# Kernel tuning notes

Measured on AMD Instinct MI355X. Metric: run time of the kernel, lower is better.

Reference implementation:

```python
import jax, jax.numpy as jnp
import numpy as np

N, E, D, A, G, S, NG = 100000, 1600000, 64, 64, 64, 4, 16


def setup_inputs() -> dict:
    key = jax.random.key(0)
    ks = jax.random.split(key, 16)
    x = jax.random.normal(ks[0], (N, D), dtype=jnp.float32)
    x_global = jax.random.normal(ks[1], (NG, G), dtype=jnp.float32)
    edge_attr = jax.random.normal(ks[2], (E, 2), dtype=jnp.float32)
    edge_index = jax.random.randint(ks[3], (2, E), 0, N, dtype=jnp.int32)
    batch_ind = jnp.sort(jax.random.randint(ks[4], (N,), 0, NG, dtype=jnp.int32))
    s = lambda fan: 1.0 / np.sqrt(fan)
    Wm = jax.random.normal(ks[5], (S, D, A), dtype=jnp.float32) * s(D)
    bm = jnp.zeros((S, A), dtype=jnp.float32)
    Wa = jax.random.normal(ks[6], (S, D + G + A, D), dtype=jnp.float32) * s(D + G + A)
    ba = jnp.zeros((S, D), dtype=jnp.float32)
    Wgate = jax.random.normal(ks[7], (S, D, 1), dtype=jnp.float32) * s(D)
    bgate = jnp.zeros((S, 1), dtype=jnp.float32)
    Wfeat = jax.random.normal(ks[8], (S, D, D), dtype=jnp.float32) * s(D)
    bfeat = jnp.zeros((S, D), dtype=jnp.float32)
    Wt = jax.random.normal(ks[9], (S, 2 * G, G), dtype=jnp.float32) * s(2 * G)
    bt = jnp.zeros((S, G), dtype=jnp.float32)
    return {
        'x': x, 'x_global': x_global, 'edge_attr': edge_attr,
        'edge_index': edge_index, 'batch_ind': batch_ind, 'num_graphs': NG,
        'Wm': Wm, 'bm': bm, 'Wa': Wa, 'ba': ba,
        'Wgate': Wgate, 'bgate': bgate, 'Wfeat': Wfeat, 'bfeat': bfeat,
        'Wt': Wt, 'bt': bt,
    }


def reference(x, x_global, edge_attr, edge_index, batch_ind, num_graphs,
              Wm, bm, Wa, ba, Wgate, bgate, Wfeat, bfeat, Wt, bt):
    lrelu = jax.nn.leaky_relu  # negative_slope=0.01, matching torch LeakyReLU
    src, dst = edge_index[0], edge_index[1]
    n_nodes = x.shape[0]
    steps = Wm.shape[0]
    for i in range(steps):
        # --- GraphNet step: gather -> edge MLP -> scatter-max ---
        msg = lrelu(x[src] @ Wm[i] + bm[i])                          # [E, A]
        agg = jax.ops.segment_max(msg, dst, num_segments=n_nodes)    # [N, A]
        agg = jnp.where(jnp.isfinite(agg), agg, 0.0)                 # empty segs -> 0
        xg_b = x_global[batch_ind]                                   # [N, G]
        z = jnp.concatenate([x, xg_b, agg], axis=1)                  # [N, D+G+A]
        x = lrelu(z @ Wa[i] + ba[i]) + x                             # residual
        # --- GlobalNode: attentional (segment-softmax) pooling ---
        gate = x @ Wgate[i] + bgate[i]                               # [N, 1]
        gmax = jax.ops.segment_max(gate, batch_ind, num_segments=num_graphs)
        e = jnp.exp(gate - gmax[batch_ind])
        denom = jax.ops.segment_sum(e, batch_ind, num_segments=num_graphs)
        alpha = e / denom[batch_ind]                                 # [N, 1]
        feat = lrelu(x @ Wfeat[i] + bfeat[i])                        # [N, D]
        xg = jax.ops.segment_sum(alpha * feat, batch_ind, num_segments=num_graphs)
        cat = jnp.concatenate([xg, x_global], axis=1)                # [NG, 2G]
        x_global = lrelu(cat @ Wt[i] + bt[i]) + x_global             # residual
    return x, x_global
```

## Files before the change

### kernel.cpp

```cpp
#include <hip/hip_runtime.h>

#define FD 64
#define NSLOPE 0.01f
#define SCAN_BS 1024

__device__ __forceinline__ float lrelu(float v) { return v > 0.f ? v : NSLOPE * v; }

__device__ __forceinline__ unsigned enc_f32(float f) {
    unsigned u = __float_as_uint(f);
    return (u & 0x80000000u) ? ~u : (u | 0x80000000u);
}
__device__ __forceinline__ float dec_f32(unsigned u) {
    return (u & 0x80000000u) ? __uint_as_float(u & 0x7FFFFFFFu) : __uint_as_float(~u);
}


__global__ void k_hist(const int* __restrict__ dst, int* __restrict__ deg, int E)
{
    int e = blockIdx.x * blockDim.x + threadIdx.x;
    if (e < E) atomicAdd(&deg[dst[e]], 1);
}

__global__ void k_scan1(const int* __restrict__ deg, int* __restrict__ off,
                        int* __restrict__ bsums, int N)
{
    __shared__ int tmp[SCAN_BS];
    int t = threadIdx.x, b = blockIdx.x;
    int i = b * SCAN_BS + t;
    int v = (i < N) ? deg[i] : 0;
    tmp[t] = v;
    __syncthreads();
    for (int d = 1; d < SCAN_BS; d <<= 1) {
        int add = (t >= d) ? tmp[t - d] : 0;
        __syncthreads();
        tmp[t] += add;
        __syncthreads();
    }
    if (i < N) off[i] = tmp[t] - v;
    if (t == SCAN_BS - 1) bsums[b] = tmp[t];
}

__global__ void k_scan2(int* __restrict__ bsums, int nb)
{
    __shared__ int tmp[SCAN_BS];
    int t = threadIdx.x;
    int v = (t < nb) ? bsums[t] : 0;
    tmp[t] = v;
    __syncthreads();
    for (int d = 1; d < SCAN_BS; d <<= 1) {
        int add = (t >= d) ? tmp[t - d] : 0;
        __syncthreads();
        tmp[t] += add;
        __syncthreads();
    }
    if (t < nb) bsums[t] = tmp[t] - v;
}

__global__ void k_scan3(int* __restrict__ off, const int* __restrict__ bsums,
                        int* __restrict__ cursor, int N)
{
    int i = blockIdx.x * blockDim.x + threadIdx.x;
    if (i < N) {
        int o = off[i] + bsums[i >> 10];
        off[i] = o;
        cursor[i] = o;
    }
}

__global__ void k_place(const int* __restrict__ src, const int* __restrict__ dst,
                        int* __restrict__ cursor, int* __restrict__ esrc, int E)
{
    int e = blockIdx.x * blockDim.x + threadIdx.x;
    if (e >= E) return;
    int pos = atomicAdd(&cursor[dst[e]], 1);
    esrc[pos] = src[e];
}


__global__ void k_proj(const float* __restrict__ x, const float* __restrict__ Wm,
                       const float* __restrict__ bm, float* __restrict__ p, int N)
{
    int n = blockIdx.x * blockDim.x + threadIdx.x;
    if (n >= N) return;
    const float* xr = x + (size_t)n * FD;
    float acc[FD];
#pragma unroll
    for (int j = 0; j < FD; ++j) acc[j] = bm[j];
    for (int kt = 0; kt < FD / 8; ++kt) {
        float4 a = *(const float4*)(xr + kt * 8);
        float4 b = *(const float4*)(xr + kt * 8 + 4);
        float z8[8] = {a.x, a.y, a.z, a.w, b.x, b.y, b.z, b.w};
#pragma unroll
        for (int kk = 0; kk < 8; ++kk) {
            const float* wrow = Wm + (kt * 8 + kk) * FD;
#pragma unroll
            for (int j = 0; j < FD; ++j) acc[j] += z8[kk] * wrow[j];
        }
    }
    float* pr = p + (size_t)n * FD;
#pragma unroll
    for (int j = 0; j < FD; ++j) pr[j] = acc[j];
}

__global__ void k_agg(const float4* __restrict__ p4, const int* __restrict__ off,
                      const int* __restrict__ endp, const int* __restrict__ esrc,
                      float4* __restrict__ agg4, int N)
{
    int tid = threadIdx.x;
    int q = tid & 15;
    int n = blockIdx.x * 16 + (tid >> 4);
    if (n >= N) return;
    int j0 = off[n], j1 = endp[n];
    float4 m = make_float4(-__builtin_inff(), -__builtin_inff(),
                           -__builtin_inff(), -__builtin_inff());
    int j = j0;
    for (; j + 1 < j1; j += 2) {
        int s0 = esrc[j], s1 = esrc[j + 1];
        float4 v0 = p4[(size_t)s0 * 16 + q];
        float4 v1 = p4[(size_t)s1 * 16 + q];
        m.x = fmaxf(m.x, v0.x); m.y = fmaxf(m.y, v0.y);
        m.z = fmaxf(m.z, v0.z); m.w = fmaxf(m.w, v0.w);
        m.x = fmaxf(m.x, v1.x); m.y = fmaxf(m.y, v1.y);
        m.z = fmaxf(m.z, v1.z); m.w = fmaxf(m.w, v1.w);
    }
    if (j < j1) {
        int s0 = esrc[j];
        float4 v0 = p4[(size_t)s0 * 16 + q];
        m.x = fmaxf(m.x, v0.x); m.y = fmaxf(m.y, v0.y);
        m.z = fmaxf(m.z, v0.z); m.w = fmaxf(m.w, v0.w);
    }
    float4 o;
    if (j0 == j1) o = make_float4(0.f, 0.f, 0.f, 0.f);
    else { o.x = lrelu(m.x); o.y = lrelu(m.y); o.z = lrelu(m.z); o.w = lrelu(m.w); }
    agg4[(size_t)n * 16 + q] = o;
}

__global__ void k_node(const float* __restrict__ x_in, float* __restrict__ x_out,
                       const float* __restrict__ xg, const int* __restrict__ batch,
                       const float* __restrict__ agg,
                       const float* __restrict__ Wa, const float* __restrict__ ba,
                       const float* __restrict__ Wgate, const float* __restrict__ bgate,
                       const float* __restrict__ Wfeat, const float* __restrict__ bfeat,
                       float* __restrict__ gate_out, float* __restrict__ feat_out,
                       unsigned* __restrict__ gmax_enc, int N)
{
    __shared__ unsigned lmax[16];
    int tid = threadIdx.x;
    if (tid < 16) lmax[tid] = 0u;
    __syncthreads();
    int n = blockIdx.x * blockDim.x + tid;
    if (n < N) {
        int g = batch[n];
        const float* xr  = x_in + (size_t)n * FD;
        const float* xgr = xg + (size_t)g * FD;
        const float* ar  = agg + (size_t)n * FD;
        float acc[FD];
#pragma unroll
        for (int j = 0; j < FD; ++j) acc[j] = ba[j];
        for (int kt = 0; kt < 8; ++kt) {
            float4 a = *(const float4*)(xr + kt * 8);
            float4 b = *(const float4*)(xr + kt * 8 + 4);
            float z8[8] = {a.x, a.y, a.z, a.w, b.x, b.y, b.z, b.w};
#pragma unroll
            for (int kk = 0; kk < 8; ++kk) {
                const float* wrow = Wa + (kt * 8 + kk) * FD;
#pragma unroll
                for (int j = 0; j < FD; ++j) acc[j] += z8[kk] * wrow[j];
            }
        }
        for (int kt = 0; kt < 8; ++kt) {
            float4 a = *(const float4*)(xgr + kt * 8);
            float4 b = *(const float4*)(xgr + kt * 8 + 4);
            float z8[8] = {a.x, a.y, a.z, a.w, b.x, b.y, b.z, b.w};
#pragma unroll
            for (int kk = 0; kk < 8; ++kk) {
                const float* wrow = Wa + (64 + kt * 8 + kk) * FD;
#pragma unroll
                for (int j = 0; j < FD; ++j) acc[j] += z8[kk] * wrow[j];
            }
        }
        for (int kt = 0; kt < 8; ++kt) {
            float4 a = *(const float4*)(ar + kt * 8);
            float4 b = *(const float4*)(ar + kt * 8 + 4);
            float z8[8] = {a.x, a.y, a.z, a.w, b.x, b.y, b.z, b.w};
#pragma unroll
            for (int kk = 0; kk < 8; ++kk) {
                const float* wrow = Wa + (128 + kt * 8 + kk) * FD;
#pragma unroll
                for (int j = 0; j < FD; ++j) acc[j] += z8[kk] * wrow[j];
            }
        }
        float gv = bgate[0];
        float* xo = x_out + (size_t)n * FD;
#pragma unroll
        for (int j = 0; j < FD; ++j) {
            float v = lrelu(acc[j]) + xr[j];
            xo[j] = v;
            gv += v * Wgate[j];
        }
        gate_out[n] = gv;
        atomicMax(&lmax[g], enc_f32(gv));
        float acc2[FD];
#pragma unroll
        for (int j = 0; j < FD; ++j) acc2[j] = bfeat[j];
        for (int kt = 0; kt < 8; ++kt) {
            float4 a = *(const float4*)(xo + kt * 8);
            float4 b = *(const float4*)(xo + kt * 8 + 4);
            float z8[8] = {a.x, a.y, a.z, a.w, b.x, b.y, b.z, b.w};
#pragma unroll
            for (int kk = 0; kk < 8; ++kk) {
                const float* wrow = Wfeat + (kt * 8 + kk) * FD;
#pragma unroll
                for (int j = 0; j < FD; ++j) acc2[j] += z8[kk] * wrow[j];
            }
        }
        float* fo = feat_out + (size_t)n * FD;
#pragma unroll
        for (int j = 0; j < FD; ++j) fo[j] = lrelu(acc2[j]);
    }
    __syncthreads();
    if (tid < 16 && lmax[tid] != 0u) atomicMax(&gmax_enc[tid], lmax[tid]);
}

__global__ void k_pool(const float* __restrict__ gate, const float* __restrict__ feat,
                       const int* __restrict__ batch, const unsigned* __restrict__ gmax_enc,
                       float* __restrict__ sum_e, float* __restrict__ Vv, int N)
{
    int gid = blockIdx.x * blockDim.x + threadIdx.x;
    int wave = gid >> 6;
    int lane = threadIdx.x & 63;
    int nwaves = (gridDim.x * blockDim.x) >> 6;
    int chunk = (N + nwaves - 1) / nwaves;
    int n0 = wave * chunk;
    int n1 = min(N, n0 + chunk);
    if (n0 >= n1) return;
    int gcur = batch[n0];
    float gm = dec_f32(gmax_enc[gcur]);
    float accv = 0.f, acce = 0.f;
    for (int n = n0; n < n1; ++n) {
        int g = batch[n];
        if (g != gcur) {
            atomicAdd(&Vv[gcur * FD + lane], accv);
            if (lane == 0) atomicAdd(&sum_e[gcur], acce);
            gcur = g;
            gm = dec_f32(gmax_enc[g]);
            accv = 0.f; acce = 0.f;
        }
        float e = __expf(gate[n] - gm);
        accv += e * feat[(size_t)n * FD + lane];
        acce += e;
    }
    atomicAdd(&Vv[gcur * FD + lane], accv);
    if (lane == 0) atomicAdd(&sum_e[gcur], acce);
}

__global__ void k_global(const float* __restrict__ xg_in, float* __restrict__ xg_out,
                         const float* __restrict__ Vv, const float* __restrict__ sum_e,
                         const float* __restrict__ Wt, const float* __restrict__ bt, int NG)
{
    __shared__ float xgn[FD], xgo[FD];
    int g = blockIdx.x, j = threadIdx.x;
    xgn[j] = Vv[g * FD + j] / sum_e[g];
    xgo[j] = xg_in[g * FD + j];
    __syncthreads();
    float acc = bt[j];
    for (int k = 0; k < FD; ++k) acc += xgn[k] * Wt[k * FD + j];
    for (int k = 0; k < FD; ++k) acc += xgo[k] * Wt[(FD + k) * FD + j];
    xg_out[g * FD + j] = lrelu(acc) + xgo[j];
}

extern "C" void kernel_launch(void* const* d_in, const int* in_sizes, int n_in,
                              void* d_out, int out_size, void* d_ws, size_t ws_size,
                              hipStream_t stream)
{
    const float* x0     = (const float*)d_in[0];
    const float* xg0    = (const float*)d_in[1];
    const int*   ei     = (const int*)d_in[3];
    const int*   batch  = (const int*)d_in[4];
    const float* Wm     = (const float*)d_in[6];
    const float* bm     = (const float*)d_in[7];
    const float* Wa     = (const float*)d_in[8];
    const float* ba     = (const float*)d_in[9];
    const float* Wgate  = (const float*)d_in[10];
    const float* bgate  = (const float*)d_in[11];
    const float* Wfeat  = (const float*)d_in[12];
    const float* bfeat  = (const float*)d_in[13];
    const float* Wt     = (const float*)d_in[14];
    const float* bt     = (const float*)d_in[15];

    const int N  = in_sizes[0] / FD;
    const int E  = in_sizes[3] / 2;
    const int NG = in_sizes[1] / FD;
    const int S  = in_sizes[6] / (FD * FD);

    const int* esrc_in = ei;
    const int* edst_in = ei + E;

    float* x_out  = (float*)d_out;
    float* xg_out = (float*)d_out + (size_t)N * FD;

    char* ws = (char*)d_ws;
    const size_t rowB = (size_t)N * FD * 4;
    float* agg   = (float*)ws;
    float* p     = (float*)(ws + rowB);
    float* feat  = p;
    int*   esrc  = (int*)(ws + 2 * rowB);
    int*   off   = (int*)(ws + 2 * rowB + (size_t)E * 4);
    int*   endp  = off + N;
    int*   deg   = endp + N;
    float* gate  = (float*)deg;
    int*   bsums = deg + N;
    unsigned* gmax_enc = (unsigned*)(bsums + 1024);
    float* sum_e = (float*)(gmax_enc + 64);
    float* Vv    = sum_e + 64;

    const int nb_node = (N + 255) / 256;
    const int nb_edge = (E + 255) / 256;
    const int nb_scan = (N + SCAN_BS - 1) / SCAN_BS;
    const int nb_agg  = (N + 15) / 16;

    hipMemsetAsync(deg, 0, (size_t)N * 4, stream);
    k_hist <<<nb_edge, 256, 0, stream>>>(edst_in, deg, E);
    k_scan1<<<nb_scan, SCAN_BS, 0, stream>>>(deg, off, bsums, N);
    k_scan2<<<1, SCAN_BS, 0, stream>>>(bsums, nb_scan);
    k_scan3<<<nb_node, 256, 0, stream>>>(off, bsums, endp, N);
    k_place<<<nb_edge, 256, 0, stream>>>(esrc_in, edst_in, endp, esrc, E);

    const float* x_in  = x0;
    const float* xg_in = xg0;

    for (int i = 0; i < S; ++i) {
        hipMemsetAsync(gmax_enc, 0, (64 + 64 + 1024) * 4, stream);
        k_proj<<<nb_node, 256, 0, stream>>>(x_in, Wm + i * FD * FD, bm + i * FD, p, N);
        k_agg <<<nb_agg, 256, 0, stream>>>((const float4*)p, off, endp, esrc,
                                           (float4*)agg, N);
        k_node<<<nb_node, 256, 0, stream>>>(x_in, x_out, xg_in, batch, agg,
                                            Wa + (size_t)i * 192 * FD, ba + i * FD,
                                            Wgate + i * FD, bgate + i,
                                            Wfeat + i * FD * FD, bfeat + i * FD,
                                            gate, feat, gmax_enc, N);
        k_pool<<<256, 256, 0, stream>>>(gate, feat, batch, gmax_enc, sum_e, Vv, N);
        k_global<<<NG, FD, 0, stream>>>(xg_in, xg_out, Vv, sum_e,
                                        Wt + (size_t)i * 2 * FD * FD, bt + i * FD, NG);
        x_in  = x_out;
        xg_in = xg_out;
    }
}
```

Before: 1.221 ms.

## Split node projections across four threads per node with float4 weight loads

k_proj and k_node now give each node to four threads, each computing 16 output columns with float4 weight loads and stores, in place of one thread computing all 64 columns. This cuts the per-thread accumulator arrays from 64 to 16 registers to raise occupancy, and makes each thread's output stores contiguous float4 writes. In k_node the residual output is kept in padded shared memory for the Wfeat matmul, and the gate dot product is reduced with shuffles across the four lanes. The cost is that x, x_global and agg rows are now read four times, once by each of the four threads.

```diff
diff --git a/kernel.cpp b/kernel.cpp
--- a/kernel.cpp
+++ b/kernel.cpp
@@ -3,6 +3,7 @@
 #define FD 64
 #define NSLOPE 0.01f
 #define SCAN_BS 1024
+#define XP_STRIDE 68
 
 __device__ __forceinline__ float lrelu(float v) { return v > 0.f ? v : NSLOPE * v; }
 
@@ -80,26 +81,36 @@
 __global__ void k_proj(const float* __restrict__ x, const float* __restrict__ Wm,
                        const float* __restrict__ bm, float* __restrict__ p, int N)
 {
-    int n = blockIdx.x * blockDim.x + threadIdx.x;
+    int t = blockIdx.x * blockDim.x + threadIdx.x;
+    int n = t >> 2, j0 = (t & 3) * 16;
     if (n >= N) return;
     const float* xr = x + (size_t)n * FD;
-    float acc[FD];
-#pragma unroll
-    for (int j = 0; j < FD; ++j) acc[j] = bm[j];
-    for (int kt = 0; kt < FD / 8; ++kt) {
+    float acc[16];
+#pragma unroll
+    for (int c = 0; c < 4; ++c) {
+        float4 b = *(const float4*)&bm[j0 + c * 4];
+        acc[c * 4 + 0] = b.x; acc[c * 4 + 1] = b.y; acc[c * 4 + 2] = b.z; acc[c * 4 + 3] = b.w;
+    }
+    for (int kt = 0; kt < 8; ++kt) {
         float4 a = *(const float4*)(xr + kt * 8);
         float4 b = *(const float4*)(xr + kt * 8 + 4);
         float z8[8] = {a.x, a.y, a.z, a.w, b.x, b.y, b.z, b.w};
 #pragma unroll
         for (int kk = 0; kk < 8; ++kk) {
-            const float* wrow = Wm + (kt * 8 + kk) * FD;
-#pragma unroll
-            for (int j = 0; j < FD; ++j) acc[j] += z8[kk] * wrow[j];
+            const float* wr = Wm + (kt * 8 + kk) * FD + j0;
+#pragma unroll
+            for (int c = 0; c < 4; ++c) {
+                float4 w = *(const float4*)(wr + c * 4);
+                acc[c * 4 + 0] += z8[kk] * w.x; acc[c * 4 + 1] += z8[kk] * w.y;
+                acc[c * 4 + 2] += z8[kk] * w.z; acc[c * 4 + 3] += z8[kk] * w.w;
+            }
         }
     }
-    float* pr = p + (size_t)n * FD;
-#pragma unroll
-    for (int j = 0; j < FD; ++j) pr[j] = acc[j];
+    float* pr = p + (size_t)n * FD + j0;
+#pragma unroll
+    for (int c = 0; c < 4; ++c)
+        *(float4*)(pr + c * 4) = make_float4(acc[c * 4 + 0], acc[c * 4 + 1],
+                                             acc[c * 4 + 2], acc[c * 4 + 3]);
 }
 
 __global__ void k_agg(const float4* __restrict__ p4, const int* __restrict__ off,
@@ -144,79 +155,97 @@
                        float* __restrict__ gate_out, float* __restrict__ feat_out,
                        unsigned* __restrict__ gmax_enc, int N)
 {
+    __shared__ float Xp[64 * XP_STRIDE];
     __shared__ unsigned lmax[16];
-    int tid = threadIdx.x;
+    const int tid = threadIdx.x;
     if (tid < 16) lmax[tid] = 0u;
-    __syncthreads();
-    int n = blockIdx.x * blockDim.x + tid;
-    if (n < N) {
-        int g = batch[n];
-        const float* xr  = x_in + (size_t)n * FD;
-        const float* xgr = xg + (size_t)g * FD;
-        const float* ar  = agg + (size_t)n * FD;
-        float acc[FD];
-#pragma unroll
-        for (int j = 0; j < FD; ++j) acc[j] = ba[j];
+
+    const int ln = tid >> 2;
+    const int q  = tid & 3;
+    const int j0 = q * 16;
+    const int n  = blockIdx.x * 64 + ln;
+    const int nc = min(n, N - 1);
+
+    const float* xr  = x_in + (size_t)nc * FD;
+    const float* xgr = xg + (size_t)batch[nc] * FD;
+    const float* ar  = agg + (size_t)nc * FD;
+
+    float acc[16];
+#pragma unroll
+    for (int c = 0; c < 4; ++c) {
+        float4 b = *(const float4*)&ba[j0 + c * 4];
+        acc[c * 4 + 0] = b.x; acc[c * 4 + 1] = b.y; acc[c * 4 + 2] = b.z; acc[c * 4 + 3] = b.w;
+    }
+
+    for (int seg = 0; seg < 3; ++seg) {
+        const float* srow = (seg == 0) ? xr : (seg == 1) ? xgr : ar;
         for (int kt = 0; kt < 8; ++kt) {
-            float4 a = *(const float4*)(xr + kt * 8);
-            float4 b = *(const float4*)(xr + kt * 8 + 4);
+            float4 a = *(const float4*)(srow + kt * 8);
+            float4 b = *(const float4*)(srow + kt * 8 + 4);
             float z8[8] = {a.x, a.y, a.z, a.w, b.x, b.y, b.z, b.w};
 #pragma unroll
             for (int kk = 0; kk < 8; ++kk) {
-                const float* wrow = Wa + (kt * 8 + kk) * FD;
-#pragma unroll
-                for (int j = 0; j < FD; ++j) acc[j] += z8[kk] * wrow[j];
+                const float* wr = Wa + (size_t)(seg * 64 + kt * 8 + kk) * FD + j0;
+#pragma unroll
+                for (int c = 0; c < 4; ++c) {
+                    float4 w = *(const float4*)(wr + c * 4);
+                    acc[c * 4 + 0] += z8[kk] * w.x; acc[c * 4 + 1] += z8[kk] * w.y;
+                    acc[c * 4 + 2] += z8[kk] * w.z; acc[c * 4 + 3] += z8[kk] * w.w;
+                }
             }
         }
-        for (int kt = 0; kt < 8; ++kt) {
-            float4 a = *(const float4*)(xgr + kt * 8);
-            float4 b = *(const float4*)(xgr + kt * 8 + 4);
-            float z8[8] = {a.x, a.y, a.z, a.w, b.x, b.y, b.z, b.w};
-#pragma unroll
-            for (int kk = 0; kk < 8; ++kk) {
-                const float* wrow = Wa + (64 + kt * 8 + kk) * FD;
-#pragma unroll
-                for (int j = 0; j < FD; ++j) acc[j] += z8[kk] * wrow[j];
+    }
+
+    float gpart = 0.f;
+    float* xo = x_out + (size_t)n * FD + j0;
+#pragma unroll
+    for (int c = 0; c < 4; ++c) {
+        float4 xv = *(const float4*)(xr + j0 + c * 4);
+        float4 wg = *(const float4*)&Wgate[j0 + c * 4];
+        float v0 = lrelu(acc[c * 4 + 0]) + xv.x;
+        float v1 = lrelu(acc[c * 4 + 1]) + xv.y;
+        float v2 = lrelu(acc[c * 4 + 2]) + xv.z;
+        float v3 = lrelu(acc[c * 4 + 3]) + xv.w;
+        *(float4*)&Xp[ln * XP_STRIDE + j0 + c * 4] = make_float4(v0, v1, v2, v3);
+        if (n < N) *(float4*)(xo + c * 4) = make_float4(v0, v1, v2, v3);
+        gpart += v0 * wg.x + v1 * wg.y + v2 * wg.z + v3 * wg.w;
+    }
+    gpart += __shfl_xor(gpart, 1);
+    gpart += __shfl_xor(gpart, 2);
+    if (q == 0 && n < N) {
+        float gv = gpart + bgate[0];
+        gate_out[n] = gv;
+        atomicMax(&lmax[batch[n]], enc_f32(gv));
+    }
+    __syncthreads();
+
+    float acc2[16];
+#pragma unroll
+    for (int c = 0; c < 4; ++c) {
+        float4 b = *(const float4*)&bfeat[j0 + c * 4];
+        acc2[c * 4 + 0] = b.x; acc2[c * 4 + 1] = b.y; acc2[c * 4 + 2] = b.z; acc2[c * 4 + 3] = b.w;
+    }
+    for (int kt = 0; kt < 8; ++kt) {
+        float4 a = *(const float4*)&Xp[ln * XP_STRIDE + kt * 8];
+        float4 b = *(const float4*)&Xp[ln * XP_STRIDE + kt * 8 + 4];
+        float z8[8] = {a.x, a.y, a.z, a.w, b.x, b.y, b.z, b.w};
+#pragma unroll
+        for (int kk = 0; kk < 8; ++kk) {
+            const float* wr = Wfeat + (size_t)(kt * 8 + kk) * FD + j0;
+#pragma unroll
+            for (int c = 0; c < 4; ++c) {
+                float4 w = *(const float4*)(wr + c * 4);
+                acc2[c * 4 + 0] += z8[kk] * w.x; acc2[c * 4 + 1] += z8[kk] * w.y;
+                acc2[c * 4 + 2] += z8[kk] * w.z; acc2[c * 4 + 3] += z8[kk] * w.w;
             }
         }
-        for (int kt = 0; kt < 8; ++kt) {
-            float4 a = *(const float4*)(ar + kt * 8);
-            float4 b = *(const float4*)(ar + kt * 8 + 4);
-            float z8[8] = {a.x, a.y, a.z, a.w, b.x, b.y, b.z, b.w};
-#pragma unroll
-            for (int kk = 0; kk < 8; ++kk) {
-                const float* wrow = Wa + (128 + kt * 8 + kk) * FD;
-#pragma unroll
-                for (int j = 0; j < FD; ++j) acc[j] += z8[kk] * wrow[j];
-            }
-        }
-        float gv = bgate[0];
-        float* xo = x_out + (size_t)n * FD;
-#pragma unroll
-        for (int j = 0; j < FD; ++j) {
-            float v = lrelu(acc[j]) + xr[j];
-            xo[j] = v;
-            gv += v * Wgate[j];
-        }
-        gate_out[n] = gv;
-        atomicMax(&lmax[g], enc_f32(gv));
-        float acc2[FD];
-#pragma unroll
-        for (int j = 0; j < FD; ++j) acc2[j] = bfeat[j];
-        for (int kt = 0; kt < 8; ++kt) {
-            float4 a = *(const float4*)(xo + kt * 8);
-            float4 b = *(const float4*)(xo + kt * 8 + 4);
-            float z8[8] = {a.x, a.y, a.z, a.w, b.x, b.y, b.z, b.w};
-#pragma unroll
-            for (int kk = 0; kk < 8; ++kk) {
-                const float* wrow = Wfeat + (kt * 8 + kk) * FD;
-#pragma unroll
-                for (int j = 0; j < FD; ++j) acc2[j] += z8[kk] * wrow[j];
-            }
-        }
-        float* fo = feat_out + (size_t)n * FD;
-#pragma unroll
-        for (int j = 0; j < FD; ++j) fo[j] = lrelu(acc2[j]);
+    }
+    if (n < N) {
+        float* fo = feat_out + (size_t)n * FD + j0;
+#pragma unroll
+        for (int c = 0; c < 4; ++c)
+            *(float4*)(fo + c * 4) = make_float4(lrelu(acc2[c * 4 + 0]), lrelu(acc2[c * 4 + 1]),
+                                                 lrelu(acc2[c * 4 + 2]), lrelu(acc2[c * 4 + 3]));
     }
     __syncthreads();
     if (tid < 16 && lmax[tid] != 0u) atomicMax(&gmax_enc[tid], lmax[tid]);
@@ -318,6 +347,8 @@
     const int nb_edge = (E + 255) / 256;
     const int nb_scan = (N + SCAN_BS - 1) / SCAN_BS;
     const int nb_agg  = (N + 15) / 16;
+    const int nb_q4   = ((N * 4) + 255) / 256;
+    const int nb_n64  = (N + 63) / 64;
 
     hipMemsetAsync(deg, 0, (size_t)N * 4, stream);
     k_hist <<<nb_edge, 256, 0, stream>>>(edst_in, deg, E);
@@ -331,14 +362,14 @@
 
     for (int i = 0; i < S; ++i) {
         hipMemsetAsync(gmax_enc, 0, (64 + 64 + 1024) * 4, stream);
-        k_proj<<<nb_node, 256, 0, stream>>>(x_in, Wm + i * FD * FD, bm + i * FD, p, N);
+        k_proj<<<nb_q4, 256, 0, stream>>>(x_in, Wm + i * FD * FD, bm + i * FD, p, N);
         k_agg <<<nb_agg, 256, 0, stream>>>((const float4*)p, off, endp, esrc,
                                            (float4*)agg, N);
-        k_node<<<nb_node, 256, 0, stream>>>(x_in, x_out, xg_in, batch, agg,
-                                            Wa + (size_t)i * 192 * FD, ba + i * FD,
-                                            Wgate + i * FD, bgate + i,
-                                            Wfeat + i * FD * FD, bfeat + i * FD,
-                                            gate, feat, gmax_enc, N);
+        k_node<<<nb_n64, 256, 0, stream>>>(x_in, x_out, xg_in, batch, agg,
+                                           Wa + (size_t)i * 192 * FD, ba + i * FD,
+                                           Wgate + i * FD, bgate + i,
+                                           Wfeat + i * FD * FD, bfeat + i * FD,
+                                           gate, feat, gmax_enc, N);
         k_pool<<<256, 256, 0, stream>>>(gate, feat, batch, gmax_enc, sum_e, Vv, N);
         k_global<<<NG, FD, 0, stream>>>(xg_in, xg_out, Vv, sum_e,
                                         Wt + (size_t)i * 2 * FD * FD, bt + i * FD, NG);
```

New measurement: 2.838 ms. +132.4%, slower.
